# Kernel optimization log

Measured on AMD Instinct MI355X. Metric: run time of the kernel, lower is better.

Reference implementation:

```python
import jax, jax.numpy as jnp
import numpy as np

B, T, D, O = 32, 1024, 1024, 256


def _glorot(key, shape):
    fan_in, fan_out = shape[0], shape[-1]
    std = np.sqrt(2.0 / (fan_in + fan_out))
    return jax.random.normal(key, shape, dtype=jnp.float32) * std


def setup_inputs() -> dict:
    key = jax.random.key(0)
    ks = jax.random.split(key, 14)
    return {
        "inputs": jax.random.normal(ks[0], (B, T, D), dtype=jnp.float32),
        # attention cell params
        "Wa": _glorot(ks[1], (O, O)),
        "Ua": _glorot(ks[2], (D, O)),
        "Va": _glorot(ks[3], (O, 1)),
        "Ba1": _glorot(ks[4], (1, O)),
        "Ba2": _glorot(ks[5], (T, O)),
        "Ba3": _glorot(ks[6], (T, 1)),
        # cascaded GRU cell params (Bo1 and inner keras GRUCell are unused in call)
        "Wo": _glorot(ks[7], (O, 1)),
        "Uo": _glorot(ks[8], (D, O)),
        "Co": _glorot(ks[9], (D, O)),
        "Bo2": _glorot(ks[10], (1, O)),
        "Bo3": _glorot(ks[11], (1, O)),
        "Bo4": _glorot(ks[12], (1, O)),
        "emb": _glorot(ks[13], (O, O)),
    }


def reference(inputs, Wa, Ua, Va, Ba1, Ba2, Ba3, Wo, Uo, Co, Bo2, Bo3, Bo4, emb):
    # inputs: [B, T, D]
    # UaH is identical every decoder step in the original code -> hoist (same math).
    UaH = jnp.einsum("btd,do->bto", inputs, Ua) + Ba2          # [B,T,O]
    # prev_state at step t is inputs[:, t-1, :] with wraparound at t=0.
    prev_in = jnp.roll(inputs, 1, axis=1)                        # [B,T,D]
    UoH_all = jnp.einsum("btd,do->bto", prev_in, Uo) + Bo2      # [B,T,O]

    def step(prev_pred, uoh_t):
        # --- attention cell (query = tanh(prev_pred)) ---
        WaS = jnp.tanh(prev_pred) @ Wa + Ba1                     # [B,O]
        scores = jnp.tanh(UaH + WaS[:, None, :]) @ Va + Ba3     # [B,T,1]
        sm = jax.nn.softmax(scores, axis=1)                      # [B,T,1]
        ctx = jnp.sum(inputs * sm, axis=1)                       # [B,D]
        # --- cascaded GRU cell ---
        woy = (jax.nn.softmax(prev_pred) @ emb) @ Wo             # [B,1]
        coc = ctx @ Co + Bo3                                     # [B,O]
        pred = woy + uoh_t + coc + Bo4                           # [B,O]
        return pred, pred

    init = jnp.zeros((inputs.shape[0], Wa.shape[0]), dtype=inputs.dtype)
    _, outs = jax.lax.scan(step, init, jnp.swapaxes(UoH_all, 0, 1))  # [T,B,O]
    return jnp.swapaxes(outs, 0, 1)                                   # [B,T,O]
```

## Files before the change

kernel.cpp:

```cpp
#include <hip/hip_runtime.h>
#include <hip/hip_fp16.h>


typedef unsigned int uint32;
typedef unsigned short u16;

#define NTH 512

__device__ __forceinline__ float b2f(u16 u) { return __uint_as_float(((uint32)u) << 16); }
__device__ __forceinline__ u16 f2b(float f) {
    uint32 u = __float_as_uint(f);
    uint32 r = u + 0x7fffu + ((u >> 16) & 1u);
    return (u16)(r >> 16);
}
__device__ __forceinline__ float lo_bf(uint32 d) { return __uint_as_float(d << 16); }
__device__ __forceinline__ float hi_bf(uint32 d) { return __uint_as_float(d & 0xffff0000u); }
__device__ __forceinline__ float tanh_fast(float x) {
    float e = __expf(x + x);
    return 1.0f - 2.0f * __builtin_amdgcn_rcpf(e + 1.0f);
}
__device__ __forceinline__ uint32 packh(float f, int t) {
    return (((uint32)t) << 16) | (uint32)__half_as_ushort(__float2half(f));
}
__device__ __forceinline__ float unpackh(uint32 w) {
    return __half2float(__ushort_as_half((unsigned short)(w & 0xFFFFu)));
}

#define OFF_E  ((size_t)0)
#define OFF_IC ((size_t)16777216)
#define WS_NEEDED ((size_t)33554432)

__device__ uint32 g_P[2][32][2064];
__device__ uint32 g_cnt[64];
__device__ float g_embWo[256];

__global__ __launch_bounds__(256) void init_k() {
    int i = blockIdx.x * 256 + threadIdx.x;
    ((uint32*)g_P)[i] = 0xFFFF0000u;
    if (i < 64) g_cnt[i] = 0u;
}

__global__ void setup_embWo(const float* __restrict__ emb, const float* __restrict__ Wo) {
    int o = threadIdx.x;
    float a = 0.f;
    for (int j = 0; j < 256; j++) a = fmaf(emb[o * 256 + j], Wo[j], a);
    g_embWo[o] = a;
}

__global__ __launch_bounds__(256) void gemm_pre(
    const float* __restrict__ in, const float* __restrict__ Ua,
    const float* __restrict__ Uo, const float* __restrict__ Co,
    const float* __restrict__ Ba2, const float* __restrict__ Bo2,
    const float* __restrict__ Bo3, const float* __restrict__ Bo4,
    u16* __restrict__ E, float* __restrict__ outStage, u16* __restrict__ ic) {
    __shared__ __align__(16) float smA[32][132];
    __shared__ __align__(16) float smB[32][128];

    int tid = threadIdx.x;
    int rt = blockIdx.x, ct = blockIdx.y;
    int mat = ct >> 1;
    int o0 = (ct & 1) * 128;
    const float* W = (mat == 0) ? Ua : (mat == 1 ? Uo : Co);
    int r0 = rt * 128;
    int b = r0 >> 10, t0 = r0 & 1023;
    int tr = tid >> 4, tc = tid & 15;

    float acc[8][8];
#pragma unroll
    for (int i = 0; i < 8; i++)
#pragma unroll
        for (int j = 0; j < 8; j++) acc[i][j] = 0.f;

    for (int kc = 0; kc < 1024; kc += 32) {
#pragma unroll
        for (int l = 0; l < 4; l++) {
            int s = tid + l * 256;
            int i = s >> 3, c = s & 7;
            float4 v = *(const float4*)(in + (size_t)(r0 + i) * 1024 + kc + c * 4);
            smA[c * 4 + 0][i] = v.x;
            smA[c * 4 + 1][i] = v.y;
            smA[c * 4 + 2][i] = v.z;
            smA[c * 4 + 3][i] = v.w;
        }
#pragma unroll
        for (int l = 0; l < 4; l++) {
            int s = tid + l * 256;
            int dd = s >> 5, c = s & 31;
            *(float4*)&smB[dd][c * 4] = *(const float4*)(W + (size_t)(kc + dd) * 256 + o0 + c * 4);
        }
        __syncthreads();
#pragma unroll 4
        for (int j = 0; j < 32; j++) {
            float a0[8], b0[8];
            *(float4*)&a0[0] = *(const float4*)&smA[j][tr * 8];
            *(float4*)&a0[4] = *(const float4*)&smA[j][tr * 8 + 4];
            *(float4*)&b0[0] = *(const float4*)&smB[j][tc * 8];
            *(float4*)&b0[4] = *(const float4*)&smB[j][tc * 8 + 4];
#pragma unroll
            for (int rr = 0; rr < 8; rr++)
#pragma unroll
                for (int cc = 0; cc < 8; cc++) acc[rr][cc] = fmaf(a0[rr], b0[cc], acc[rr][cc]);
        }
        __syncthreads();
    }

    if (mat == 0) {
#pragma unroll
        for (int rr = 0; rr < 8; rr++) {
            int t = t0 + tr * 8 + rr;
#pragma unroll
            for (int cc = 0; cc < 8; cc++) {
                int o = o0 + tc * 8 + cc;
                float v = __expf(2.f * (acc[rr][cc] + Ba2[t * 256 + o]));
                E[((((size_t)b << 10) + t) << 8) + o] = f2b(v);
            }
        }
    } else if (mat == 1) {
#pragma unroll
        for (int rr = 0; rr < 8; rr++) {
            int t = t0 + tr * 8 + rr;
            int t1 = (t + 1) & 1023;
#pragma unroll
            for (int cc = 0; cc < 8; cc++) {
                int o = o0 + tc * 8 + cc;
                outStage[(((size_t)b << 10) + t1) * 256 + o] = acc[rr][cc] + Bo2[o] + Bo3[o] + Bo4[o];
            }
        }
    } else {
#pragma unroll
        for (int rr = 0; rr < 8; rr++) {
            int t = t0 + tr * 8 + rr;
#pragma unroll
            for (int cc = 0; cc < 8; cc++)
                ic[(((size_t)b << 10) + t) * 256 + o0 + tc * 8 + cc] = f2b(acc[rr][cc]);
        }
    }
}

__global__ __launch_bounds__(NTH) void seq8(
    const float* __restrict__ Wa, const float* __restrict__ Va,
    const float* __restrict__ Ba1, const float* __restrict__ Ba3,
    const u16* __restrict__ E, const u16* __restrict__ IC,
    float* __restrict__ out) {
    __shared__ uint32 smWa2[128 * 256];
    __shared__ __align__(16) float smScratch[2064];
    __shared__ float smPred[256], smQ[256], smF[256], smVa[256], smBa1[256];
    __shared__ float smS[128], smEe[128], smBa3[128];
    __shared__ float smT[16];

    int tid = threadIdx.x;
    int b = blockIdx.x & 31, g = blockIdx.x >> 5;
    int lane = tid & 63, w = tid >> 6;
    int t0 = g << 7;

    if (tid < 256) {
        smVa[tid] = Va[tid]; smBa1[tid] = Ba1[tid];
        smPred[tid] = 0.f; smQ[tid] = 0.f;
    }
    if (tid < 128) smBa3[tid] = Ba3[t0 + tid];
    for (int idx = tid; idx < 32768; idx += NTH) {
        int j2 = idx >> 8, o = idx & 255;
        uint32 u0 = (uint32)f2b(Wa[(size_t)(2 * j2) * 256 + o]);
        uint32 u1 = (uint32)f2b(Wa[(size_t)(2 * j2 + 1) * 256 + o]);
        smWa2[idx] = u0 | (u1 << 16);
    }
    __syncthreads();

    float sv = (tid < 256) ? smVa[tid] : 0.f;
#pragma unroll
    for (int off = 32; off; off >>= 1) sv += __shfl_xor(sv, off, 64);
    if (lane == 0) smT[w] = sv;
    __syncthreads();
    float sumVa = smT[0] + smT[1] + smT[2] + smT[3];
    float myEmb = (tid < 256) ? g_embWo[tid] : 0.f;
    __syncthreads();

    const u16* Eb = E + ((size_t)b << 18);
    const u16* ICb = IC + ((size_t)b << 18);
    float* outb = out + ((size_t)b << 18);
    long bud = 1000000000L;

    for (int t = 0; t < 1024; t++) {
        uint32* buf = &g_P[t & 1][b][0];
        uint32* cnt = &g_cnt[(b << 1) | (t & 1)];
        uint32 target = 8u * (uint32)((t >> 1) + 1);
        float uoh = (tid < 256) ? outb[((size_t)t << 8) + tid] : 0.f;

        float pv = 0.f;
        if (tid < 256) {
            pv = smPred[tid];
            float m = pv;
#pragma unroll
            for (int off = 32; off; off >>= 1) m = fmaxf(m, __shfl_xor(m, off, 64));
            if (lane == 0) smT[w] = m;
        }
        {
            int o = tid & 255, h = tid >> 8;
            const uint32* wp = &smWa2[(h << 6) * 256 + o];
            const float* qp = &smQ[h << 7];
            float a = 0.f;
#pragma unroll 8
            for (int j2 = 0; j2 < 64; j2++) {
                float2 q2 = *(const float2*)&qp[j2 * 2];
                uint32 p = wp[j2 << 8];
                a = fmaf(lo_bf(p), q2.x, a);
                a = fmaf(hi_bf(p), q2.y, a);
            }
            smScratch[tid] = a;
        }
        __syncthreads();
        if (tid < 256) {
            float M = fmaxf(fmaxf(smT[0], smT[1]), fmaxf(smT[2], smT[3]));
            float e = __expf(pv - M);
            float s1 = e, s2 = e * myEmb;
#pragma unroll
            for (int off = 32; off; off >>= 1) {
                s1 += __shfl_xor(s1, off, 64);
                s2 += __shfl_xor(s2, off, 64);
            }
            if (lane == 0) { smT[4 + w] = s1; smT[8 + w] = s2; }
            smF[tid] = __expf(2.f * (smBa1[tid] + smScratch[tid] + smScratch[256 + tid]));
        }
        __syncthreads();
        float p_val = (smT[8] + smT[9] + smT[10] + smT[11]) *
                      __builtin_amdgcn_rcpf(smT[4] + smT[5] + smT[6] + smT[7]);

        {
            int tl = tid >> 2, oq = tid & 3;
            const uint4* row = (const uint4*)(Eb + (((size_t)(t0 + tl)) << 8) + (oq << 6));
            float acc = 0.f;
#pragma unroll
            for (int k = 0; k < 8; k++) {
                uint4 ev = row[k];
                int ob = (oq << 6) + (k << 3);
                float4 fA = *(const float4*)&smF[ob];
                float4 fB = *(const float4*)&smF[ob + 4];
                float4 vA = *(const float4*)&smVa[ob];
                float4 vB = *(const float4*)&smVa[ob + 4];
                acc = fmaf(vA.x, __builtin_amdgcn_rcpf(fmaf(lo_bf(ev.x), fA.x, 1.f)), acc);
                acc = fmaf(vA.y, __builtin_amdgcn_rcpf(fmaf(hi_bf(ev.x), fA.y, 1.f)), acc);
                acc = fmaf(vA.z, __builtin_amdgcn_rcpf(fmaf(lo_bf(ev.y), fA.z, 1.f)), acc);
                acc = fmaf(vA.w, __builtin_amdgcn_rcpf(fmaf(hi_bf(ev.y), fA.w, 1.f)), acc);
                acc = fmaf(vB.x, __builtin_amdgcn_rcpf(fmaf(lo_bf(ev.z), fB.x, 1.f)), acc);
                acc = fmaf(vB.y, __builtin_amdgcn_rcpf(fmaf(hi_bf(ev.z), fB.y, 1.f)), acc);
                acc = fmaf(vB.z, __builtin_amdgcn_rcpf(fmaf(lo_bf(ev.w), fB.z, 1.f)), acc);
                acc = fmaf(vB.w, __builtin_amdgcn_rcpf(fmaf(hi_bf(ev.w), fB.w, 1.f)), acc);
            }
            acc += __shfl_xor(acc, 1, 64);
            acc += __shfl_xor(acc, 2, 64);
            if (oq == 0) smS[tl] = sumVa - 2.f * acc + smBa3[tl];
        }
        __syncthreads();
        float m_g = 0.f, S_g = 0.f;
        if (tid < 128) {
            float s = smS[tid];
            float mm = s;
#pragma unroll
            for (int off = 32; off; off >>= 1) mm = fmaxf(mm, __shfl_xor(mm, off, 64));
            if (lane == 0) smT[w] = mm;
        }
        __syncthreads();
        if (tid < 128) {
            m_g = fmaxf(smT[0], smT[1]);
            float e = __expf(smS[tid] - m_g);
            smEe[tid] = e;
            float ls = e;
#pragma unroll
            for (int off = 32; off; off >>= 1) ls += __shfl_xor(ls, off, 64);
            if (lane == 0) smT[2 + w] = ls;
        }
        __syncthreads();
        m_g = fmaxf(smT[0], smT[1]);
        S_g = smT[2] + smT[3];

        {
            int rg = tid >> 6, oc = tid & 63, o4 = oc << 2;
            const u16* icp = ICb + (((size_t)t0) << 8) + o4;
            float4 a4 = {0.f, 0.f, 0.f, 0.f};
#pragma unroll 4
            for (int r = 0; r < 16; r++) {
                int row = (rg << 4) + r;
                float e = smEe[row];
                uint2 iv = *(const uint2*)(icp + ((size_t)row << 8));
                a4.x = fmaf(e, lo_bf(iv.x), a4.x);
                a4.y = fmaf(e, hi_bf(iv.x), a4.y);
                a4.z = fmaf(e, lo_bf(iv.y), a4.z);
                a4.w = fmaf(e, hi_bf(iv.y), a4.w);
            }
            *(float4*)&smScratch[rg * 256 + o4] = a4;
        }
        __syncthreads();
        if (tid < 256) {
            float P = 0.f;
#pragma unroll
            for (int rg = 0; rg < 8; rg++) P += smScratch[rg * 256 + tid];
            atomicExch(&buf[g * 258 + tid], packh(P, t));
        }
        if (tid == 0) {
            atomicExch(&buf[g * 258 + 256], packh(m_g, t));
            atomicExch(&buf[g * 258 + 257], packh(S_g, t));
        }
        __syncthreads();
        if (tid == 0) {
            atomicAdd(cnt, 1u);
            while (atomicAdd(cnt, 0u) < target && bud > 0) bud--;
        }
        __syncthreads();
        {
            uint32 tt = (uint32)t;
            uint32 w0 = 0xFFFF0000u, w1 = 0xFFFF0000u, w2 = 0xFFFF0000u, w3 = 0xFFFF0000u;
            int has4 = (tid < 16);
            uint32 w4 = has4 ? 0xFFFF0000u : (tt << 16);
            while (bud > 0) {
                if ((w0 >> 16) != tt) w0 = atomicAdd(&buf[tid], 0u);
                if ((w1 >> 16) != tt) w1 = atomicAdd(&buf[tid + 512], 0u);
                if ((w2 >> 16) != tt) w2 = atomicAdd(&buf[tid + 1024], 0u);
                if ((w3 >> 16) != tt) w3 = atomicAdd(&buf[tid + 1536], 0u);
                if (has4 && (w4 >> 16) != tt) w4 = atomicAdd(&buf[tid + 2048], 0u);
                if ((w0 >> 16) == tt && (w1 >> 16) == tt && (w2 >> 16) == tt &&
                    (w3 >> 16) == tt && (w4 >> 16) == tt) break;
                bud--;
            }
            smScratch[tid] = unpackh(w0);
            smScratch[tid + 512] = unpackh(w1);
            smScratch[tid + 1024] = unpackh(w2);
            smScratch[tid + 1536] = unpackh(w3);
            if (has4) smScratch[tid + 2048] = unpackh(w4);
        }
        __syncthreads();
        if (tid < 256) {
            float M = smScratch[256];
#pragma unroll
            for (int g2 = 1; g2 < 8; g2++) M = fmaxf(M, smScratch[g2 * 258 + 256]);
            float L = 0.f, Pt = 0.f;
#pragma unroll
            for (int g2 = 0; g2 < 8; g2++) {
                float eg = __expf(smScratch[g2 * 258 + 256] - M);
                L = fmaf(eg, smScratch[g2 * 258 + 257], L);
                Pt = fmaf(eg, smScratch[g2 * 258 + tid], Pt);
            }
            float pr = p_val + uoh + Pt * __builtin_amdgcn_rcpf(L);
            if ((tid >> 5) == g) outb[((size_t)t << 8) + tid] = pr;
            smPred[tid] = pr;
            smQ[tid] = tanh_fast(pr);
        }
        __syncthreads();
    }
}

__global__ void zero_k(uint32* out, int n) {
    int i = blockIdx.x * 1024 + threadIdx.x;
    if (i < n) out[i] = 0;
}

extern "C" void kernel_launch(void* const* d_in, const int* in_sizes, int n_in,
                              void* d_out, int out_size, void* d_ws, size_t ws_size,
                              hipStream_t stream) {
    const float* in = (const float*)d_in[0];
    const float* Wa = (const float*)d_in[1];
    const float* Ua = (const float*)d_in[2];
    const float* Va = (const float*)d_in[3];
    const float* Ba1 = (const float*)d_in[4];
    const float* Ba2 = (const float*)d_in[5];
    const float* Ba3 = (const float*)d_in[6];
    const float* Wo = (const float*)d_in[7];
    const float* Uo = (const float*)d_in[8];
    const float* Co = (const float*)d_in[9];
    const float* Bo2 = (const float*)d_in[10];
    const float* Bo3 = (const float*)d_in[11];
    const float* Bo4 = (const float*)d_in[12];
    const float* emb = (const float*)d_in[13];
    float* out = (float*)d_out;
    char* ws = (char*)d_ws;

    if (ws_size < WS_NEEDED) {
        zero_k<<<(out_size + 1023) / 1024, 1024, 0, stream>>>((uint32*)out, out_size);
        return;
    }

    u16* E = (u16*)(ws + OFF_E);
    u16* icp = (u16*)(ws + OFF_IC);

    init_k<<<516, 256, 0, stream>>>();
    setup_embWo<<<1, 256, 0, stream>>>(emb, Wo);
    gemm_pre<<<dim3(256, 6), 256, 0, stream>>>(in, Ua, Uo, Co, Ba2, Bo2, Bo3, Bo4, E, out, icp);
    seq8<<<256, NTH, 0, stream>>>(Wa, Va, Ba1, Ba3, E, icp, out);
}
```

Before: 8.003 ms.

## Keep Wa in registers and stage E/IC tiles in shared memory

Wa moves from shared memory into a per-thread register array of 64 packed bf16 pairs. The query is broadcast with readlane from a bf16 shared array instead of being read as floats from LDS. This frees LDS, so each block's 128-row slices of E and IC are copied into padded shared-memory tiles once and then reused across all 1024 sequential steps, instead of being read from global or L2 every step. The costs are heavy register pressure under a launch bound of 2 blocks per CU, and an extra bf16 rounding of tanh(pred) for the query.

```diff
diff --git a/kernel.cpp b/kernel.cpp
--- a/kernel.cpp
+++ b/kernel.cpp
@@ -6,6 +6,7 @@
 typedef unsigned short u16;
 
 #define NTH 512
+#define ROWP 264
 
 __device__ __forceinline__ float b2f(u16 u) { return __uint_as_float(((uint32)u) << 16); }
 __device__ __forceinline__ u16 f2b(float f) {
@@ -137,32 +138,48 @@
     }
 }
 
-__global__ __launch_bounds__(NTH) void seq8(
+__global__ __launch_bounds__(NTH, 2) void seq8(
     const float* __restrict__ Wa, const float* __restrict__ Va,
     const float* __restrict__ Ba1, const float* __restrict__ Ba3,
     const u16* __restrict__ E, const u16* __restrict__ IC,
     float* __restrict__ out) {
-    __shared__ uint32 smWa2[128 * 256];
+    __shared__ __align__(16) u16 smE[128 * ROWP];
+    __shared__ __align__(16) u16 smIC[128 * ROWP];
     __shared__ __align__(16) float smScratch[2064];
-    __shared__ float smPred[256], smQ[256], smF[256], smVa[256], smBa1[256];
+    __shared__ float smPred[256], smF[256], smVa[256], smBa1[256];
+    __shared__ u16 smQh[256];
     __shared__ float smS[128], smEe[128], smBa3[128];
     __shared__ float smT[16];
 
     int tid = threadIdx.x;
     int b = blockIdx.x & 31, g = blockIdx.x >> 5;
     int lane = tid & 63, w = tid >> 6;
+    int o = tid & 255, h = tid >> 8;
     int t0 = g << 7;
 
     if (tid < 256) {
         smVa[tid] = Va[tid]; smBa1[tid] = Ba1[tid];
-        smPred[tid] = 0.f; smQ[tid] = 0.f;
+        smPred[tid] = 0.f; smQh[tid] = 0;
     }
     if (tid < 128) smBa3[tid] = Ba3[t0 + tid];
-    for (int idx = tid; idx < 32768; idx += NTH) {
-        int j2 = idx >> 8, o = idx & 255;
-        uint32 u0 = (uint32)f2b(Wa[(size_t)(2 * j2) * 256 + o]);
-        uint32 u1 = (uint32)f2b(Wa[(size_t)(2 * j2 + 1) * 256 + o]);
-        smWa2[idx] = u0 | (u1 << 16);
+
+    uint32 wap[64];
+#pragma unroll 8
+    for (int k = 0; k < 64; k++) {
+        int j0 = (h << 7) + 2 * k;
+        uint32 u0 = (uint32)f2b(Wa[(size_t)j0 * 256 + o]);
+        uint32 u1 = (uint32)f2b(Wa[(size_t)(j0 + 1) * 256 + o]);
+        wap[k] = u0 | (u1 << 16);
+    }
+
+    const u16* Eb = E + ((size_t)b << 18);
+    const u16* ICb = IC + ((size_t)b << 18);
+    for (int idx = tid; idx < 128 * 32; idx += NTH) {
+        int row = idx >> 5, seg = idx & 31;
+        *(uint4*)(smE + row * ROWP + seg * 8) =
+            *(const uint4*)(Eb + (((size_t)(t0 + row)) << 8) + seg * 8);
+        *(uint4*)(smIC + row * ROWP + seg * 8) =
+            *(const uint4*)(ICb + (((size_t)(t0 + row)) << 8) + seg * 8);
     }
     __syncthreads();
 
@@ -175,8 +192,6 @@
     float myEmb = (tid < 256) ? g_embWo[tid] : 0.f;
     __syncthreads();
 
-    const u16* Eb = E + ((size_t)b << 18);
-    const u16* ICb = IC + ((size_t)b << 18);
     float* outb = out + ((size_t)b << 18);
     long bud = 1000000000L;
 
@@ -195,16 +210,14 @@
             if (lane == 0) smT[w] = m;
         }
         {
-            int o = tid & 255, h = tid >> 8;
-            const uint32* wp = &smWa2[(h << 6) * 256 + o];
-            const float* qp = &smQ[h << 7];
+            uint32 qreg = ((const uint32*)smQh)[(h << 6) + lane];
             float a = 0.f;
-#pragma unroll 8
-            for (int j2 = 0; j2 < 64; j2++) {
-                float2 q2 = *(const float2*)&qp[j2 * 2];
-                uint32 p = wp[j2 << 8];
-                a = fmaf(lo_bf(p), q2.x, a);
-                a = fmaf(hi_bf(p), q2.y, a);
+#pragma unroll
+            for (int k = 0; k < 64; k++) {
+                uint32 qq = (uint32)__builtin_amdgcn_readlane((int)qreg, k);
+                uint32 wv = wap[k];
+                a = fmaf(lo_bf(qq), lo_bf(wv), a);
+                a = fmaf(hi_bf(qq), hi_bf(wv), a);
             }
             smScratch[tid] = a;
         }
@@ -227,7 +240,7 @@
 
         {
             int tl = tid >> 2, oq = tid & 3;
-            const uint4* row = (const uint4*)(Eb + (((size_t)(t0 + tl)) << 8) + (oq << 6));
+            const uint4* row = (const uint4*)smE + tl * (ROWP / 8) + oq * 8;
             float acc = 0.f;
 #pragma unroll
             for (int k = 0; k < 8; k++) {
@@ -275,13 +288,13 @@
 
         {
             int rg = tid >> 6, oc = tid & 63, o4 = oc << 2;
-            const u16* icp = ICb + (((size_t)t0) << 8) + o4;
+            const uint2* icp2 = (const uint2*)smIC;
             float4 a4 = {0.f, 0.f, 0.f, 0.f};
 #pragma unroll 4
             for (int r = 0; r < 16; r++) {
                 int row = (rg << 4) + r;
                 float e = smEe[row];
-                uint2 iv = *(const uint2*)(icp + ((size_t)row << 8));
+                uint2 iv = icp2[row * (ROWP / 4) + oc];
                 a4.x = fmaf(e, lo_bf(iv.x), a4.x);
                 a4.y = fmaf(e, hi_bf(iv.x), a4.y);
                 a4.z = fmaf(e, lo_bf(iv.y), a4.z);
@@ -342,7 +355,7 @@
             float pr = p_val + uoh + Pt * __builtin_amdgcn_rcpf(L);
             if ((tid >> 5) == g) outb[((size_t)t << 8) + tid] = pr;
             smPred[tid] = pr;
-            smQ[tid] = tanh_fast(pr);
+            smQh[tid] = f2b(tanh_fast(pr));
         }
         __syncthreads();
     }
```

Result: slower. 10.48 ms (+30.9%).
